# Kernel tuning notes

Hardware: AMD Instinct MI355X
Metric: run time of the kernel (lower is better)

## Reference

```python
import jax, jax.numpy as jnp
import numpy as np

B, HW, N, C, F, ITERS = 32, 4096, 16, 128, 512, 3
EPS_LN = 1e-5
EPS_ATTN = 1e-5


def _ln(x, g, b):
    m = x.mean(-1, keepdims=True)
    v = ((x - m) ** 2).mean(-1, keepdims=True)
    return (x - m) / jnp.sqrt(v + EPS_LN) * g + b


def _gru(x, h, wih, whh, bih, bhh):
    # torch.nn.GRUCell math
    gi = x @ wih.T + bih
    gh = h @ whh.T + bhh
    i_r, i_z, i_n = jnp.split(gi, 3, axis=-1)
    h_r, h_z, h_n = jnp.split(gh, 3, axis=-1)
    r = jax.nn.sigmoid(i_r + h_r)
    z = jax.nn.sigmoid(i_z + h_z)
    n = jnp.tanh(i_n + r * h_n)
    return (1.0 - z) * n + z * h


def setup_inputs() -> dict:
    key = jax.random.key(0)
    ks = jax.random.split(key, 16)
    s = 0.02
    d = {
        'inp': jax.random.normal(ks[0], (B, HW, C), jnp.float32),
        'query': jax.random.normal(ks[1], (B, N, C), jnp.float32),
        'ln_kv_g': jnp.ones((C,), jnp.float32),
        'ln_kv_b': jnp.zeros((C,), jnp.float32),
        'Wk': jax.random.normal(ks[2], (C, C), jnp.float32) * s,
        'Wv': jax.random.normal(ks[3], (C, C), jnp.float32) * s,
        'ln_q_g': jnp.ones((C,), jnp.float32),
        'ln_q_b': jnp.zeros((C,), jnp.float32),
        'Wq': jax.random.normal(ks[4], (C, C), jnp.float32) * s,
        'gru_wih': jax.random.normal(ks[5], (3 * C, C), jnp.float32) * s,
        'gru_whh': jax.random.normal(ks[6], (3 * C, C), jnp.float32) * s,
        'gru_bih': jnp.zeros((3 * C,), jnp.float32),
        'gru_bhh': jnp.zeros((3 * C,), jnp.float32),
        'ln2_g': jnp.ones((C,), jnp.float32),
        'ln2_b': jnp.zeros((C,), jnp.float32),
        'ffn_w1': jax.random.normal(ks[7], (F, C), jnp.float32) * s,
        'ffn_b1': jnp.zeros((F,), jnp.float32),
        'ffn_w2': jax.random.normal(ks[8], (C, F), jnp.float32) * s,
        'ffn_b2': jnp.zeros((C,), jnp.float32),
    }
    return d


def reference(inp, query, ln_kv_g, ln_kv_b, Wk, Wv, ln_q_g, ln_q_b, Wq,
              gru_wih, gru_whh, gru_bih, gru_bhh, ln2_g, ln2_b,
              ffn_w1, ffn_b1, ffn_w2, ffn_b2):
    b, n, c = query.shape
    kv = _ln(inp, ln_kv_g, ln_kv_b)
    k = kv @ Wk.T  # (b, hw, c)
    v = kv @ Wv.T  # (b, hw, c)
    scale = c ** -0.5
    q = query
    a0 = None
    for _ in range(ITERS):
        x = q
        qn = _ln(q, ln_q_g, ln_q_b) @ Wq.T
        logit = jnp.einsum('bqc,bkc->bqk', qn * scale, k)  # (b, n, hw)
        a0 = jax.nn.softmax(logit, axis=1)  # inverted: softmax over slots
        a = a0 / (a0.sum(2, keepdims=True) + EPS_ATTN)  # renorm over keys
        u = jnp.einsum('bqk,bkc->bqc', a, v)
        y = _gru(u.reshape(b * n, c), x.reshape(b * n, c),
                 gru_wih, gru_whh, gru_bih, gru_bhh).reshape(b, n, c)
        z = _ln(y, ln2_g, ln2_b)
        ffn = jax.nn.relu(z @ ffn_w1.T + ffn_b1) @ ffn_w2.T + ffn_b2
        q = y + ffn
    return (q, a0)
```

## Files before the change

kernel.cpp:

```cpp
#include <hip/hip_runtime.h>
#include <math.h>

#define B_ 32
#define HW_ 4096
#define N_ 16
#define C_ 128
#define F_ 512
#define ITERS_ 3
#define EPS_LN 1e-5f
#define EPS_ATTN 1e-5f

typedef __attribute__((ext_vector_type(8))) short short8;
typedef __attribute__((ext_vector_type(4))) float f32x4;

static __device__ __forceinline__ unsigned short f2b(float f) {
    union { float f; unsigned u; } v; v.f = f;
    unsigned r = v.u + 0x7fffu + ((v.u >> 16) & 1u);
    return (unsigned short)(r >> 16);
}
static __device__ __forceinline__ float blo(unsigned u) {
    union { unsigned u; float f; } v; v.u = u << 16; return v.f;
}
static __device__ __forceinline__ float bhi(unsigned u) {
    union { unsigned u; float f; } v; v.u = u & 0xffff0000u; return v.f;
}

__global__ __launch_bounds__(256) void k_wprep(
    const float* __restrict__ Wk, const float* __restrict__ Wv,
    const float* __restrict__ wih, const float* __restrict__ whh,
    const float* __restrict__ w1, const float* __restrict__ w2,
    unsigned short* __restrict__ Wk_bf, unsigned short* __restrict__ Wv_bf,
    unsigned short* __restrict__ wih_bf, unsigned short* __restrict__ whh_bf,
    unsigned short* __restrict__ w1_bf, unsigned short* __restrict__ w2_bf)
{
    int t = blockIdx.x * 256 + threadIdx.x;
    const float* src; unsigned short* dst; int off;
    if (t < 4096)       { src = Wk;  dst = Wk_bf;  off = t; }
    else if (t < 8192)  { src = Wv;  dst = Wv_bf;  off = t - 4096; }
    else if (t < 20480) { src = wih; dst = wih_bf; off = t - 8192; }
    else if (t < 32768) { src = whh; dst = whh_bf; off = t - 20480; }
    else if (t < 49152) { src = w1;  dst = w1_bf;  off = t - 32768; }
    else                { src = w2;  dst = w2_bf;  off = t - 49152; }
    float4 a = ((const float4*)src)[off];
    unsigned lo = (unsigned)f2b(a.x) | ((unsigned)f2b(a.y) << 16);
    unsigned hi = (unsigned)f2b(a.z) | ((unsigned)f2b(a.w) << 16);
    uint2 p; p.x = lo; p.y = hi;
    *(uint2*)(dst + off * 4) = p;
}

__global__ __launch_bounds__(256) void k_qprep0(
    const float* __restrict__ query, const float* __restrict__ lng,
    const float* __restrict__ lnb, const float* __restrict__ Wq,
    unsigned short* __restrict__ qn_g)
{
    __shared__ __align__(16) float xq[16 * 128];
    int b = blockIdx.x, tid = threadIdx.x;
    int n = tid >> 4, part = tid & 15;
    int row = b * 16 + n;
    const float4* x4 = (const float4*)(query + row * 128 + part * 8);
    float4 x0 = x4[0], x1 = x4[1];
    float s = x0.x + x0.y + x0.z + x0.w + x1.x + x1.y + x1.z + x1.w;
    float ss = x0.x * x0.x + x0.y * x0.y + x0.z * x0.z + x0.w * x0.w +
               x1.x * x1.x + x1.y * x1.y + x1.z * x1.z + x1.w * x1.w;
    s += __shfl_xor(s, 1); s += __shfl_xor(s, 2); s += __shfl_xor(s, 4); s += __shfl_xor(s, 8);
    ss += __shfl_xor(ss, 1); ss += __shfl_xor(ss, 2); ss += __shfl_xor(ss, 4); ss += __shfl_xor(ss, 8);
    float mean = s * (1.f / 128.f);
    float var = ss * (1.f / 128.f) - mean * mean;
    float rstd = rsqrtf(var + EPS_LN);
    const float4* g4 = (const float4*)(lng + part * 8);
    const float4* b4 = (const float4*)(lnb + part * 8);
    float4 g0 = g4[0], g1 = g4[1], bb0 = b4[0], bb1 = b4[1];
    float4 o0, o1;
    o0.x = (x0.x - mean) * rstd * g0.x + bb0.x;
    o0.y = (x0.y - mean) * rstd * g0.y + bb0.y;
    o0.z = (x0.z - mean) * rstd * g0.z + bb0.z;
    o0.w = (x0.w - mean) * rstd * g0.w + bb0.w;
    o1.x = (x1.x - mean) * rstd * g1.x + bb1.x;
    o1.y = (x1.y - mean) * rstd * g1.y + bb1.y;
    o1.z = (x1.z - mean) * rstd * g1.z + bb1.z;
    o1.w = (x1.w - mean) * rstd * g1.w + bb1.w;
    float4* xrow = (float4*)&xq[n * 128];
    xrow[part * 2] = o0;
    xrow[part * 2 + 1] = o1;
    __syncthreads();
    float o[8] = {0.f, 0.f, 0.f, 0.f, 0.f, 0.f, 0.f, 0.f};
    const float4* xv4 = (const float4*)&xq[n * 128];
#pragma unroll 4
    for (int j = 0; j < 32; j++) {
        float4 xv = xv4[j];
#pragma unroll
        for (int i = 0; i < 8; i++) {
            float4 w = ((const float4*)(Wq + (part * 8 + i) * 128))[j];
            o[i] += w.x * xv.x + w.y * xv.y + w.z * xv.z + w.w * xv.w;
        }
    }
    const float scale = 0.08838834764831845f;
#pragma unroll
    for (int i = 0; i < 8; i++)
        qn_g[row * 128 + part * 8 + i] = f2b(o[i] * scale);
}

__global__ __launch_bounds__(256) void k_kvproj(
    const float* __restrict__ inp, const float* __restrict__ lng,
    const float* __restrict__ lnb, const unsigned short* __restrict__ Wk_bf,
    const unsigned short* __restrict__ Wv_bf, unsigned short* __restrict__ Kbf,
    unsigned short* __restrict__ Vt)
{
    __shared__ __align__(16) unsigned short W_lds[128 * 128];
    __shared__ __align__(16) unsigned short T_lds[64 * 136];
    const int tid = threadIdx.x;
    const int wave = tid >> 6, lane = tid & 63;
    const int l15 = lane & 15, q4 = lane >> 4;
    const int kof = q4 * 8;
    const int tile0 = blockIdx.x * 64;
    const int b = tile0 >> 12;
    const int hwbase = tile0 & (HW_ - 1);

    const int srow = tid >> 1, shalf = tid & 1;
    const int sswz = srow & 7;

    float x[4][8];
    {
        const float* rowp = inp + (tile0 + (wave << 4) + l15) * C_;
        float s = 0.f, ss = 0.f;
#pragma unroll
        for (int ks = 0; ks < 4; ks++) {
#pragma unroll
            for (int h = 0; h < 2; h++) {
                float4 v = *(const float4*)(rowp + ks * 32 + kof + h * 4);
                x[ks][h * 4 + 0] = v.x; x[ks][h * 4 + 1] = v.y;
                x[ks][h * 4 + 2] = v.z; x[ks][h * 4 + 3] = v.w;
                s += v.x + v.y + v.z + v.w;
                ss += v.x * v.x + v.y * v.y + v.z * v.z + v.w * v.w;
            }
        }
        s += __shfl_xor(s, 16);  s += __shfl_xor(s, 32);
        ss += __shfl_xor(ss, 16); ss += __shfl_xor(ss, 32);
        float mean = s * (1.f / 128.f);
        float var = ss * (1.f / 128.f) - mean * mean;
        float rstd = rsqrtf(var + EPS_LN);
#pragma unroll
        for (int ks = 0; ks < 4; ks++) {
#pragma unroll
            for (int h = 0; h < 2; h++) {
                float4 g = *(const float4*)(lng + ks * 32 + kof + h * 4);
                float4 bb = *(const float4*)(lnb + ks * 32 + kof + h * 4);
                x[ks][h * 4 + 0] = (x[ks][h * 4 + 0] - mean) * rstd * g.x + bb.x;
                x[ks][h * 4 + 1] = (x[ks][h * 4 + 1] - mean) * rstd * g.y + bb.y;
                x[ks][h * 4 + 2] = (x[ks][h * 4 + 2] - mean) * rstd * g.z + bb.z;
                x[ks][h * 4 + 3] = (x[ks][h * 4 + 3] - mean) * rstd * g.w + bb.w;
            }
        }
    }
    short8 af[4];
#pragma unroll
    for (int ks = 0; ks < 4; ks++) {
        union { short8 s8; unsigned u[4]; } p;
#pragma unroll
        for (int j = 0; j < 4; j++)
            p.u[j] = (unsigned)f2b(x[ks][2 * j]) | ((unsigned)f2b(x[ks][2 * j + 1]) << 16);
        af[ks] = p.s8;
    }

    {
        const uint4* gW = (const uint4*)Wk_bf;
#pragma unroll
        for (int j = 0; j < 8; j++) {
            int c = shalf * 8 + j;
            uint4 w = gW[srow * 16 + c];
            *(uint4*)&W_lds[srow * 128 + (c ^ sswz) * 8] = w;
        }
    }
    __syncthreads();

    f32x4 acc[8];
#pragma unroll
    for (int nt = 0; nt < 8; nt++) {
        acc[nt] = (f32x4){0.f, 0.f, 0.f, 0.f};
#pragma unroll
        for (int ks = 0; ks < 4; ks++) {
            short8 bf = *(const short8*)&W_lds[(nt * 16 + l15) * 128 + ((ks * 4 + q4) ^ (l15 & 7)) * 8];
            acc[nt] = __builtin_amdgcn_mfma_f32_16x16x32_bf16(af[ks], bf, acc[nt], 0, 0, 0);
        }
    }
#pragma unroll
    for (int nt = 0; nt < 8; nt++) {
        int c = nt * 16 + l15;
#pragma unroll
        for (int i = 0; i < 4; i++)
            T_lds[((wave << 4) + (q4 << 2) + i) * 136 + c] = f2b(acc[nt][i]);
    }
    __syncthreads();
    {
        int row = tid >> 2, part = tid & 3;
        uint4 v0 = *(const uint4*)&T_lds[row * 136 + part * 32];
        uint4 v1 = *(const uint4*)&T_lds[row * 136 + part * 32 + 8];
        uint4* dst = (uint4*)&Kbf[(b * HW_ + hwbase + row) * C_ + part * 32];
        dst[0] = v0;
        dst[1] = v1;
    }
    {
        const uint4* gW = (const uint4*)Wv_bf;
#pragma unroll
        for (int j = 0; j < 8; j++) {
            int c = shalf * 8 + j;
            uint4 w = gW[srow * 16 + c];
            *(uint4*)&W_lds[srow * 128 + (c ^ sswz) * 8] = w;
        }
    }
    __syncthreads();
#pragma unroll
    for (int nt = 0; nt < 8; nt++) {
        acc[nt] = (f32x4){0.f, 0.f, 0.f, 0.f};
#pragma unroll
        for (int ks = 0; ks < 4; ks++) {
            short8 bf = *(const short8*)&W_lds[(nt * 16 + l15) * 128 + ((ks * 4 + q4) ^ (l15 & 7)) * 8];
            acc[nt] = __builtin_amdgcn_mfma_f32_16x16x32_bf16(af[ks], bf, acc[nt], 0, 0, 0);
        }
    }
#pragma unroll
    for (int nt = 0; nt < 8; nt++) {
        int c = nt * 16 + l15;
#pragma unroll
        for (int i = 0; i < 4; i++)
            T_lds[((wave << 4) + (q4 << 2) + i) * 136 + c] = f2b(acc[nt][i]);
    }
    __syncthreads();
    {
        int c = tid >> 1, half = tid & 1;
        unsigned short* vbase = Vt + (b * C_ + c) * HW_ + hwbase + half * 32;
#pragma unroll
        for (int g = 0; g < 4; g++) {
            union { uint4 u4; unsigned u[4]; } p;
#pragma unroll
            for (int d = 0; d < 4; d++) {
                int h = half * 32 + g * 8 + d * 2;
                unsigned lo = T_lds[h * 136 + c];
                unsigned hi = T_lds[(h + 1) * 136 + c];
                p.u[d] = lo | (hi << 16);
            }
            *(uint4*)(vbase + g * 8) = p.u4;
        }
    }
}

__global__ __launch_bounds__(256) void k_attn(
    const unsigned short* __restrict__ qn_g, const unsigned short* __restrict__ Kbf,
    const unsigned short* __restrict__ Vt, float* __restrict__ Upart,
    float* __restrict__ rspart, float* __restrict__ a0_out, int last)
{
    __shared__ __align__(16) float Ul[4][2048];
    __shared__ __align__(16) unsigned short Pb[4][16 * 40];
    __shared__ float rsw[4][16];
    const int b = blockIdx.y, chunk = blockIdx.x;
    const int tid = threadIdx.x;
    const int wave = tid >> 6, lane = tid & 63;
    const int l15 = lane & 15, q4 = lane >> 4;
    const int kof = q4 * 8;
    const int hwb = chunk * 128 + wave * 32;

    short8 aq[4];
#pragma unroll
    for (int ks = 0; ks < 4; ks++)
        aq[ks] = *(const short8*)&qn_g[(b * 16 + l15) * 128 + ks * 32 + kof];

    unsigned short* Pw = &Pb[wave][0];
    float rs[4] = {0.f, 0.f, 0.f, 0.f};
#pragma unroll
    for (int s = 0; s < 2; s++) {
        int hwt = hwb + s * 16;
        f32x4 sa = {0.f, 0.f, 0.f, 0.f};
#pragma unroll
        for (int ks = 0; ks < 4; ks++) {
            short8 bk = *(const short8*)&Kbf[(b * HW_ + hwt + l15) * C_ + ks * 32 + kof];
            sa = __builtin_amdgcn_mfma_f32_16x16x32_bf16(aq[ks], bk, sa, 0, 0, 0);
        }
        float mx = fmaxf(fmaxf(sa[0], sa[1]), fmaxf(sa[2], sa[3]));
        mx = fmaxf(mx, __shfl_xor(mx, 16));
        mx = fmaxf(mx, __shfl_xor(mx, 32));
        float e[4]; float ssum = 0.f;
#pragma unroll
        for (int i = 0; i < 4; i++) { e[i] = __expf(sa[i] - mx); ssum += e[i]; }
        ssum += __shfl_xor(ssum, 16);
        ssum += __shfl_xor(ssum, 32);
        float inv = 1.f / ssum;
#pragma unroll
        for (int i = 0; i < 4; i++) {
            float a0v = e[i] * inv;
            rs[i] += a0v;
            if (last) a0_out[(b * 16 + q4 * 4 + i) * HW_ + hwt + l15] = a0v;
            Pw[(q4 * 4 + i) * 40 + s * 16 + l15] = f2b(a0v);
        }
    }
#pragma unroll
    for (int i = 0; i < 4; i++) {
        rs[i] += __shfl_xor(rs[i], 1);
        rs[i] += __shfl_xor(rs[i], 2);
        rs[i] += __shfl_xor(rs[i], 4);
        rs[i] += __shfl_xor(rs[i], 8);
    }
    if (l15 == 0) {
#pragma unroll
        for (int i = 0; i < 4; i++) rsw[wave][q4 * 4 + i] = rs[i];
    }
    short8 bp = *(const short8*)&Pw[l15 * 40 + kof];
#pragma unroll
    for (int ct = 0; ct < 8; ct++) {
        short8 av = *(const short8*)&Vt[(b * C_ + ct * 16 + l15) * HW_ + hwb + kof];
        f32x4 ua = __builtin_amdgcn_mfma_f32_16x16x32_bf16(av, bp, (f32x4){0.f, 0.f, 0.f, 0.f}, 0, 0, 0);
        int c = ct * 16 + q4 * 4;
#pragma unroll
        for (int i = 0; i < 4; i++)
            Ul[wave][(c + i) * 16 + l15] = ua[i];
    }
    __syncthreads();
    {
        float* up = Upart + (b * 32 + chunk) * 2048;
#pragma unroll
        for (int k = 0; k < 8; k++) {
            int idx = tid + k * 256;
            up[idx] = Ul[0][idx] + Ul[1][idx] + Ul[2][idx] + Ul[3][idx];
        }
        if (tid < 16)
            rspart[(b * 32 + chunk) * 16 + tid] =
                rsw[0][tid] + rsw[1][tid] + rsw[2][tid] + rsw[3][tid];
    }
}

__global__ __launch_bounds__(256) void k_tail(
    const float* __restrict__ Upart, const float* __restrict__ rspart,
    const float* __restrict__ hsrc, float* __restrict__ q_buf,
    const unsigned short* __restrict__ wih_bf, const unsigned short* __restrict__ whh_bf,
    const float* __restrict__ bih, const float* __restrict__ bhh,
    const float* __restrict__ ln2g, const float* __restrict__ ln2b,
    const unsigned short* __restrict__ w1_bf, const float* __restrict__ b1,
    const unsigned short* __restrict__ w2_bf, const float* __restrict__ b2,
    const float* __restrict__ lnqg, const float* __restrict__ lnqb,
    const float* __restrict__ Wq, unsigned short* __restrict__ qn_g,
    float* __restrict__ out_q, int last)
{
    __shared__ __align__(16) float u_l[2][128];
    __shared__ __align__(16) float h_l[2][128];
    __shared__ __align__(16) float g_l[2][768];
    __shared__ __align__(16) float z_l[2][128];
    __shared__ __align__(16) float y_l[2][128];
    __shared__ __align__(16) float h1_l[2][512];
    __shared__ float stats[2][2];
    __shared__ float wpart[4][2];
    int tid = threadIdx.x;
    int row0 = blockIdx.x * 2;
    int r = tid >> 7, c = tid & 127;
    int row = row0 + r;
    {
        int bb = row >> 4, q = row & 15;
        float rsv = 0.f, uraw = 0.f;
#pragma unroll
        for (int ch = 0; ch < 32; ch++) {
            rsv  += rspart[(bb * 32 + ch) * 16 + q];
            uraw += Upart[(bb * 32 + ch) * 2048 + c * 16 + q];
        }
        u_l[r][c] = uraw / (rsv + EPS_ATTN);
        h_l[r][c] = hsrc[row * 128 + c];
    }
    __syncthreads();
#pragma unroll
    for (int o3 = 0; o3 < 3; o3++) {
        int o = tid + o3 * 256;
        const unsigned short* wrow;
        const float* srcbase;
        float bias;
        if (o < 384) { wrow = wih_bf + o * 128; srcbase = &u_l[0][0]; bias = bih[o]; }
        else         { wrow = whh_bf + (o - 384) * 128; srcbase = &h_l[0][0]; bias = bhh[o - 384]; }
        const uint4* w4 = (const uint4*)wrow;
        const float4* s0 = (const float4*)srcbase;
        const float4* s1 = (const float4*)(srcbase + 128);
        float a0acc = 0.f, a1acc = 0.f;
#pragma unroll 8
        for (int j = 0; j < 16; j++) {
            uint4 w = w4[j];
            float w0 = blo(w.x), w1v = bhi(w.x), w2v = blo(w.y), w3 = bhi(w.y);
            float w4v = blo(w.z), w5 = bhi(w.z), w6 = blo(w.w), w7 = bhi(w.w);
            float4 aA = s0[2 * j], aB = s0[2 * j + 1];
            float4 bA = s1[2 * j], bB = s1[2 * j + 1];
            a0acc += w0 * aA.x + w1v * aA.y + w2v * aA.z + w3 * aA.w
                   + w4v * aB.x + w5 * aB.y + w6 * aB.z + w7 * aB.w;
            a1acc += w0 * bA.x + w1v * bA.y + w2v * bA.z + w3 * bA.w
                   + w4v * bB.x + w5 * bB.y + w6 * bB.z + w7 * bB.w;
        }
        g_l[0][o] = a0acc + bias;
        g_l[1][o] = a1acc + bias;
    }
    __syncthreads();
    {
        float ir = g_l[r][c], iz = g_l[r][128 + c], in_ = g_l[r][256 + c];
        float hr = g_l[r][384 + c], hz = g_l[r][512 + c], hn = g_l[r][640 + c];
        float rr = 1.f / (1.f + expf(-(ir + hr)));
        float zz = 1.f / (1.f + expf(-(iz + hz)));
        float nn = tanhf(in_ + rr * hn);
        y_l[r][c] = (1.f - zz) * nn + zz * h_l[r][c];
    }
    __syncthreads();
    if (tid < 128) {
        int w = tid >> 6, ln = tid & 63;
        float v0 = y_l[w][ln], v1 = y_l[w][ln + 64];
        float s = v0 + v1, ss = v0 * v0 + v1 * v1;
#pragma unroll
        for (int off = 1; off < 64; off <<= 1) {
            s += __shfl_xor(s, off);
            ss += __shfl_xor(ss, off);
        }
        if (ln == 0) {
            float mean = s * (1.f / 128.f);
            float var = ss * (1.f / 128.f) - mean * mean;
            stats[w][0] = mean;
            stats[w][1] = rsqrtf(var + EPS_LN);
        }
    }
    __syncthreads();
    z_l[r][c] = (y_l[r][c] - stats[r][0]) * stats[r][1] * ln2g[c] + ln2b[c];
    __syncthreads();
#pragma unroll
    for (int f2i = 0; f2i < 2; f2i++) {
        int f = tid + f2i * 256;
        const uint4* w4 = (const uint4*)(w1_bf + f * 128);
        const float4* s0 = (const float4*)&z_l[0][0];
        const float4* s1 = (const float4*)&z_l[1][0];
        float a0acc = 0.f, a1acc = 0.f;
#pragma unroll 8
        for (int j = 0; j < 16; j++) {
            uint4 w = w4[j];
            float w0 = blo(w.x), w1v = bhi(w.x), w2v = blo(w.y), w3 = bhi(w.y);
            float w4v = blo(w.z), w5 = bhi(w.z), w6 = blo(w.w), w7 = bhi(w.w);
            float4 aA = s0[2 * j], aB = s0[2 * j + 1];
            float4 bA = s1[2 * j], bB = s1[2 * j + 1];
            a0acc += w0 * aA.x + w1v * aA.y + w2v * aA.z + w3 * aA.w
                   + w4v * aB.x + w5 * aB.y + w6 * aB.z + w7 * aB.w;
            a1acc += w0 * bA.x + w1v * bA.y + w2v * bA.z + w3 * bA.w
                   + w4v * bB.x + w5 * bB.y + w6 * bB.z + w7 * bB.w;
        }
        float bv = b1[f];
        h1_l[0][f] = fmaxf(a0acc + bv, 0.f);
        h1_l[1][f] = fmaxf(a1acc + bv, 0.f);
    }
    __syncthreads();
    float q_new;
    {
        const uint4* w4 = (const uint4*)(w2_bf + c * 512);
        const float4* hh = (const float4*)&h1_l[r][0];
        float acc = 0.f;
#pragma unroll 8
        for (int j = 0; j < 64; j++) {
            uint4 w = w4[j];
            float4 hA = hh[2 * j], hB = hh[2 * j + 1];
            acc += blo(w.x) * hA.x + bhi(w.x) * hA.y + blo(w.y) * hA.z + bhi(w.y) * hA.w
                 + blo(w.z) * hB.x + bhi(w.z) * hB.y + blo(w.w) * hB.z + bhi(w.w) * hB.w;
        }
        q_new = y_l[r][c] + acc + b2[c];
        q_buf[row * 128 + c] = q_new;
        if (last) out_q[row * 128 + c] = q_new;
    }
    if (!last) {
        __syncthreads();
        y_l[r][c] = q_new;
        __syncthreads();
        {
            int w = tid >> 6, ln = tid & 63;
            float v = y_l[w >> 1][(w & 1) * 64 + ln];
            float s = v, ss = v * v;
#pragma unroll
            for (int off = 1; off < 64; off <<= 1) {
                s += __shfl_xor(s, off);
                ss += __shfl_xor(ss, off);
            }
            if (ln == 0) { wpart[w][0] = s; wpart[w][1] = ss; }
        }
        __syncthreads();
        {
            float s = wpart[2 * r][0] + wpart[2 * r + 1][0];
            float ss = wpart[2 * r][1] + wpart[2 * r + 1][1];
            float mean = s * (1.f / 128.f);
            float var = ss * (1.f / 128.f) - mean * mean;
            float rstd = rsqrtf(var + EPS_LN);
            z_l[r][c] = (q_new - mean) * rstd * lnqg[c] + lnqb[c];
        }
        __syncthreads();
        {
            const float4* w4 = (const float4*)(Wq + c * 128);
            const float4* zz = (const float4*)&z_l[r][0];
            float acc = 0.f;
#pragma unroll 8
            for (int j = 0; j < 32; j++) {
                float4 w = w4[j], v = zz[j];
                acc += w.x * v.x + w.y * v.y + w.z * v.z + w.w * v.w;
            }
            qn_g[row * 128 + c] = f2b(acc * 0.08838834764831845f);
        }
    }
}

extern "C" void kernel_launch(void* const* d_in, const int* in_sizes, int n_in,
                              void* d_out, int out_size, void* d_ws, size_t ws_size,
                              hipStream_t stream) {
    const float* inp     = (const float*)d_in[0];
    const float* query   = (const float*)d_in[1];
    const float* ln_kv_g = (const float*)d_in[2];
    const float* ln_kv_b = (const float*)d_in[3];
    const float* Wk      = (const float*)d_in[4];
    const float* Wv      = (const float*)d_in[5];
    const float* ln_q_g  = (const float*)d_in[6];
    const float* ln_q_b  = (const float*)d_in[7];
    const float* Wq      = (const float*)d_in[8];
    const float* gru_wih = (const float*)d_in[9];
    const float* gru_whh = (const float*)d_in[10];
    const float* gru_bih = (const float*)d_in[11];
    const float* gru_bhh = (const float*)d_in[12];
    const float* ln2_g   = (const float*)d_in[13];
    const float* ln2_b   = (const float*)d_in[14];
    const float* ffn_w1  = (const float*)d_in[15];
    const float* ffn_b1  = (const float*)d_in[16];
    const float* ffn_w2  = (const float*)d_in[17];
    const float* ffn_b2  = (const float*)d_in[18];

    char* ws = (char*)d_ws;
    unsigned short* Kbf    = (unsigned short*)ws;
    unsigned short* Vt     = (unsigned short*)(ws + 33554432);
    float* q_buf           = (float*)(ws + 67108864);
    float* Upart           = (float*)(ws + 67371008);
    float* rspart          = (float*)(ws + 75759616);
    unsigned short* qn_g   = (unsigned short*)(ws + 75825152);
    unsigned short* Wk_bf  = (unsigned short*)(ws + 75956224);
    unsigned short* Wv_bf  = (unsigned short*)(ws + 75988992);
    unsigned short* wih_bf = (unsigned short*)(ws + 76021760);
    unsigned short* whh_bf = (unsigned short*)(ws + 76120064);
    unsigned short* w1_bf  = (unsigned short*)(ws + 76218368);
    unsigned short* w2_bf  = (unsigned short*)(ws + 76349440);

    float* out_q  = (float*)d_out;
    float* out_a0 = out_q + B_ * N_ * C_;

    k_wprep<<<dim3(256), dim3(256), 0, stream>>>(
        Wk, Wv, gru_wih, gru_whh, ffn_w1, ffn_w2,
        Wk_bf, Wv_bf, wih_bf, whh_bf, w1_bf, w2_bf);
    k_qprep0<<<dim3(B_), dim3(256), 0, stream>>>(query, ln_q_g, ln_q_b, Wq, qn_g);
    k_kvproj<<<dim3((B_ * HW_) / 64), dim3(256), 0, stream>>>(
        inp, ln_kv_g, ln_kv_b, Wk_bf, Wv_bf, Kbf, Vt);

    for (int it = 0; it < ITERS_; it++) {
        int last = (it == ITERS_ - 1) ? 1 : 0;
        const float* hsrc = (it == 0) ? query : q_buf;
        k_attn<<<dim3(32, B_), dim3(256), 0, stream>>>(
            qn_g, Kbf, Vt, Upart, rspart, out_a0, last);
        k_tail<<<dim3((B_ * N_) / 2), dim3(256), 0, stream>>>(
            Upart, rspart, hsrc, q_buf, wih_bf, whh_bf, gru_bih, gru_bhh,
            ln2_g, ln2_b, w1_bf, ffn_b1, w2_bf, ffn_b2,
            ln_q_g, ln_q_b, Wq, qn_g, out_q, last);
    }
}
```

Before: 342.3 us.

## Merge prep kernels, transpose V via LDS, prefetch V in attention, one row per tail block

Fuses the weight-conversion and initial query-projection kernels into one launch. In the KV projection, V is now staged in LDS already transposed, so the Vt store uses vector copies instead of gathering scalar 16-bit values. The K staging uses a different row pitch. The attention kernel loads its V fragments before the score computation and reuses the U buffer for P, which drops an LDS array. The tail kernel now gives each block a single row, doubling the grid, and splits reductions across both halves of the block. This adds parallelism but also adds extra barriers and reads each weight matrix twice as often.

```diff
diff --git a/kernel.cpp b/kernel.cpp
--- a/kernel.cpp
+++ b/kernel.cpp
@@ -25,36 +25,36 @@
     union { unsigned u; float f; } v; v.u = u & 0xffff0000u; return v.f;
 }
 
-__global__ __launch_bounds__(256) void k_wprep(
+__global__ __launch_bounds__(256) void k_prep(
     const float* __restrict__ Wk, const float* __restrict__ Wv,
     const float* __restrict__ wih, const float* __restrict__ whh,
     const float* __restrict__ w1, const float* __restrict__ w2,
     unsigned short* __restrict__ Wk_bf, unsigned short* __restrict__ Wv_bf,
     unsigned short* __restrict__ wih_bf, unsigned short* __restrict__ whh_bf,
-    unsigned short* __restrict__ w1_bf, unsigned short* __restrict__ w2_bf)
-{
-    int t = blockIdx.x * 256 + threadIdx.x;
-    const float* src; unsigned short* dst; int off;
-    if (t < 4096)       { src = Wk;  dst = Wk_bf;  off = t; }
-    else if (t < 8192)  { src = Wv;  dst = Wv_bf;  off = t - 4096; }
-    else if (t < 20480) { src = wih; dst = wih_bf; off = t - 8192; }
-    else if (t < 32768) { src = whh; dst = whh_bf; off = t - 20480; }
-    else if (t < 49152) { src = w1;  dst = w1_bf;  off = t - 32768; }
-    else                { src = w2;  dst = w2_bf;  off = t - 49152; }
-    float4 a = ((const float4*)src)[off];
-    unsigned lo = (unsigned)f2b(a.x) | ((unsigned)f2b(a.y) << 16);
-    unsigned hi = (unsigned)f2b(a.z) | ((unsigned)f2b(a.w) << 16);
-    uint2 p; p.x = lo; p.y = hi;
-    *(uint2*)(dst + off * 4) = p;
-}
-
-__global__ __launch_bounds__(256) void k_qprep0(
-    const float* __restrict__ query, const float* __restrict__ lng,
-    const float* __restrict__ lnb, const float* __restrict__ Wq,
+    unsigned short* __restrict__ w1_bf, unsigned short* __restrict__ w2_bf,
+    const float* __restrict__ query, const float* __restrict__ lnqg,
+    const float* __restrict__ lnqb, const float* __restrict__ Wq,
     unsigned short* __restrict__ qn_g)
 {
     __shared__ __align__(16) float xq[16 * 128];
-    int b = blockIdx.x, tid = threadIdx.x;
+    int tid = threadIdx.x;
+    if (blockIdx.x < 256) {
+        int t = blockIdx.x * 256 + tid;
+        const float* src; unsigned short* dst; int off;
+        if (t < 4096)       { src = Wk;  dst = Wk_bf;  off = t; }
+        else if (t < 8192)  { src = Wv;  dst = Wv_bf;  off = t - 4096; }
+        else if (t < 20480) { src = wih; dst = wih_bf; off = t - 8192; }
+        else if (t < 32768) { src = whh; dst = whh_bf; off = t - 20480; }
+        else if (t < 49152) { src = w1;  dst = w1_bf;  off = t - 32768; }
+        else                { src = w2;  dst = w2_bf;  off = t - 49152; }
+        float4 a = ((const float4*)src)[off];
+        uint2 p;
+        p.x = (unsigned)f2b(a.x) | ((unsigned)f2b(a.y) << 16);
+        p.y = (unsigned)f2b(a.z) | ((unsigned)f2b(a.w) << 16);
+        *(uint2*)(dst + off * 4) = p;
+        return;
+    }
+    int b = blockIdx.x - 256;
     int n = tid >> 4, part = tid & 15;
     int row = b * 16 + n;
     const float4* x4 = (const float4*)(query + row * 128 + part * 8);
@@ -67,8 +67,8 @@
     float mean = s * (1.f / 128.f);
     float var = ss * (1.f / 128.f) - mean * mean;
     float rstd = rsqrtf(var + EPS_LN);
-    const float4* g4 = (const float4*)(lng + part * 8);
-    const float4* b4 = (const float4*)(lnb + part * 8);
+    const float4* g4 = (const float4*)(lnqg + part * 8);
+    const float4* b4 = (const float4*)(lnqb + part * 8);
     float4 g0 = g4[0], g1 = g4[1], bb0 = b4[0], bb1 = b4[1];
     float4 o0, o1;
     o0.x = (x0.x - mean) * rstd * g0.x + bb0.x;
@@ -107,7 +107,7 @@
     unsigned short* __restrict__ Vt)
 {
     __shared__ __align__(16) unsigned short W_lds[128 * 128];
-    __shared__ __align__(16) unsigned short T_lds[64 * 136];
+    __shared__ __align__(16) unsigned short T_lds[8960];
     const int tid = threadIdx.x;
     const int wave = tid >> 6, lane = tid & 63;
     const int l15 = lane & 15, q4 = lane >> 4;
@@ -188,16 +188,15 @@
         int c = nt * 16 + l15;
 #pragma unroll
         for (int i = 0; i < 4; i++)
-            T_lds[((wave << 4) + (q4 << 2) + i) * 136 + c] = f2b(acc[nt][i]);
+            T_lds[((wave << 4) + (q4 << 2) + i) * 132 + c] = f2b(acc[nt][i]);
     }
     __syncthreads();
     {
         int row = tid >> 2, part = tid & 3;
-        uint4 v0 = *(const uint4*)&T_lds[row * 136 + part * 32];
-        uint4 v1 = *(const uint4*)&T_lds[row * 136 + part * 32 + 8];
         uint4* dst = (uint4*)&Kbf[(b * HW_ + hwbase + row) * C_ + part * 32];
-        dst[0] = v0;
-        dst[1] = v1;
+#pragma unroll
+        for (int j = 0; j < 4; j++)
+            dst[j] = *(const uint4*)&T_lds[row * 132 + part * 32 + j * 8];
     }
     {
         const uint4* gW = (const uint4*)Wv_bf;
@@ -218,29 +217,21 @@
             acc[nt] = __builtin_amdgcn_mfma_f32_16x16x32_bf16(af[ks], bf, acc[nt], 0, 0, 0);
         }
     }
+    __syncthreads();
 #pragma unroll
     for (int nt = 0; nt < 8; nt++) {
         int c = nt * 16 + l15;
 #pragma unroll
         for (int i = 0; i < 4; i++)
-            T_lds[((wave << 4) + (q4 << 2) + i) * 136 + c] = f2b(acc[nt][i]);
+            T_lds[c * 70 + (wave << 4) + (q4 << 2) + i] = f2b(acc[nt][i]);
     }
     __syncthreads();
     {
         int c = tid >> 1, half = tid & 1;
-        unsigned short* vbase = Vt + (b * C_ + c) * HW_ + hwbase + half * 32;
-#pragma unroll
-        for (int g = 0; g < 4; g++) {
-            union { uint4 u4; unsigned u[4]; } p;
-#pragma unroll
-            for (int d = 0; d < 4; d++) {
-                int h = half * 32 + g * 8 + d * 2;
-                unsigned lo = T_lds[h * 136 + c];
-                unsigned hi = T_lds[(h + 1) * 136 + c];
-                p.u[d] = lo | (hi << 16);
-            }
-            *(uint4*)(vbase + g * 8) = p.u4;
-        }
+        uint4* dst = (uint4*)&Vt[(b * C_ + c) * HW_ + hwbase + half * 32];
+#pragma unroll
+        for (int j = 0; j < 4; j++)
+            dst[j] = *(const uint4*)&T_lds[c * 70 + half * 32 + j * 8];
     }
 }
 
@@ -250,7 +241,6 @@
     float* __restrict__ rspart, float* __restrict__ a0_out, int last)
 {
     __shared__ __align__(16) float Ul[4][2048];
-    __shared__ __align__(16) unsigned short Pb[4][16 * 40];
     __shared__ float rsw[4][16];
     const int b = blockIdx.y, chunk = blockIdx.x;
     const int tid = threadIdx.x;
@@ -259,12 +249,17 @@
     const int kof = q4 * 8;
     const int hwb = chunk * 128 + wave * 32;
 
+    unsigned short* Pw = (unsigned short*)&Ul[wave][0];
+
     short8 aq[4];
 #pragma unroll
     for (int ks = 0; ks < 4; ks++)
         aq[ks] = *(const short8*)&qn_g[(b * 16 + l15) * 128 + ks * 32 + kof];
-
-    unsigned short* Pw = &Pb[wave][0];
+    short8 av[8];
+#pragma unroll
+    for (int ct = 0; ct < 8; ct++)
+        av[ct] = *(const short8*)&Vt[(b * C_ + ct * 16 + l15) * HW_ + hwb + kof];
+
     float rs[4] = {0.f, 0.f, 0.f, 0.f};
 #pragma unroll
     for (int s = 0; s < 2; s++) {
@@ -306,8 +301,7 @@
     short8 bp = *(const short8*)&Pw[l15 * 40 + kof];
 #pragma unroll
     for (int ct = 0; ct < 8; ct++) {
-        short8 av = *(const short8*)&Vt[(b * C_ + ct * 16 + l15) * HW_ + hwb + kof];
-        f32x4 ua = __builtin_amdgcn_mfma_f32_16x16x32_bf16(av, bp, (f32x4){0.f, 0.f, 0.f, 0.f}, 0, 0, 0);
+        f32x4 ua = __builtin_amdgcn_mfma_f32_16x16x32_bf16(av[ct], bp, (f32x4){0.f, 0.f, 0.f, 0.f}, 0, 0, 0);
         int c = ct * 16 + q4 * 4;
 #pragma unroll
         for (int i = 0; i < 4; i++)
@@ -339,162 +333,164 @@
     const float* __restrict__ Wq, unsigned short* __restrict__ qn_g,
     float* __restrict__ out_q, int last)
 {
-    __shared__ __align__(16) float u_l[2][128];
-    __shared__ __align__(16) float h_l[2][128];
-    __shared__ __align__(16) float g_l[2][768];
-    __shared__ __align__(16) float z_l[2][128];
-    __shared__ __align__(16) float y_l[2][128];
-    __shared__ __align__(16) float h1_l[2][512];
-    __shared__ float stats[2][2];
-    __shared__ float wpart[4][2];
-    int tid = threadIdx.x;
-    int row0 = blockIdx.x * 2;
-    int r = tid >> 7, c = tid & 127;
-    int row = row0 + r;
-    {
-        int bb = row >> 4, q = row & 15;
-        float rsv = 0.f, uraw = 0.f;
-#pragma unroll
-        for (int ch = 0; ch < 32; ch++) {
-            rsv  += rspart[(bb * 32 + ch) * 16 + q];
-            uraw += Upart[(bb * 32 + ch) * 2048 + c * 16 + q];
-        }
-        u_l[r][c] = uraw / (rsv + EPS_ATTN);
-        h_l[r][c] = hsrc[row * 128 + c];
-    }
+    __shared__ __align__(16) float u_l[128];
+    __shared__ __align__(16) float h_l[128];
+    __shared__ __align__(16) float g_l[768];
+    __shared__ __align__(16) float z_l[128];
+    __shared__ __align__(16) float y_l[128];
+    __shared__ __align__(16) float h1_l[512];
+    __shared__ __align__(16) float red[256];
+    __shared__ float stats[2];
+    __shared__ float srs;
+    const int tid = threadIdx.x;
+    const int row = blockIdx.x;
+    const int b = row >> 4, q = row & 15;
+    const int lane = tid & 63;
+
+    {
+        int c = tid & 127, h = tid >> 7;
+        float part = 0.f;
+#pragma unroll
+        for (int ch = 0; ch < 16; ch++)
+            part += Upart[(b * 32 + h * 16 + ch) * 2048 + c * 16 + q];
+        red[tid] = part;
+        if (tid < 128) h_l[tid] = hsrc[row * 128 + tid];
+        if (tid < 64) {
+            float v = (lane < 32) ? rspart[(b * 32 + lane) * 16 + q] : 0.f;
+#pragma unroll
+            for (int off = 1; off < 64; off <<= 1) v += __shfl_xor(v, off);
+            if (tid == 0) srs = v;
+        }
+    }
+    __syncthreads();
+    if (tid < 128)
+        u_l[tid] = (red[tid] + red[tid + 128]) / (srs + EPS_ATTN);
     __syncthreads();
 #pragma unroll
     for (int o3 = 0; o3 < 3; o3++) {
         int o = tid + o3 * 256;
         const unsigned short* wrow;
-        const float* srcbase;
+        const float* src;
         float bias;
-        if (o < 384) { wrow = wih_bf + o * 128; srcbase = &u_l[0][0]; bias = bih[o]; }
-        else         { wrow = whh_bf + (o - 384) * 128; srcbase = &h_l[0][0]; bias = bhh[o - 384]; }
+        if (o < 384) { wrow = wih_bf + o * 128; src = u_l; bias = bih[o]; }
+        else         { wrow = whh_bf + (o - 384) * 128; src = h_l; bias = bhh[o - 384]; }
         const uint4* w4 = (const uint4*)wrow;
-        const float4* s0 = (const float4*)srcbase;
-        const float4* s1 = (const float4*)(srcbase + 128);
-        float a0acc = 0.f, a1acc = 0.f;
+        const float4* s4 = (const float4*)src;
+        float acc = 0.f;
 #pragma unroll 8
         for (int j = 0; j < 16; j++) {
             uint4 w = w4[j];
-            float w0 = blo(w.x), w1v = bhi(w.x), w2v = blo(w.y), w3 = bhi(w.y);
-            float w4v = blo(w.z), w5 = bhi(w.z), w6 = blo(w.w), w7 = bhi(w.w);
-            float4 aA = s0[2 * j], aB = s0[2 * j + 1];
-            float4 bA = s1[2 * j], bB = s1[2 * j + 1];
-            a0acc += w0 * aA.x + w1v * aA.y + w2v * aA.z + w3 * aA.w
-                   + w4v * aB.x + w5 * aB.y + w6 * aB.z + w7 * aB.w;
-            a1acc += w0 * bA.x + w1v * bA.y + w2v * bA.z + w3 * bA.w
-                   + w4v * bB.x + w5 * bB.y + w6 * bB.z + w7 * bB.w;
-        }
-        g_l[0][o] = a0acc + bias;
-        g_l[1][o] = a1acc + bias;
-    }
-    __syncthreads();
-    {
-        float ir = g_l[r][c], iz = g_l[r][128 + c], in_ = g_l[r][256 + c];
-        float hr = g_l[r][384 + c], hz = g_l[r][512 + c], hn = g_l[r][640 + c];
+            float4 aA = s4[2 * j], aB = s4[2 * j + 1];
+            acc += blo(w.x) * aA.x + bhi(w.x) * aA.y + blo(w.y) * aA.z + bhi(w.y) * aA.w
+                 + blo(w.z) * aB.x + bhi(w.z) * aB.y + blo(w.w) * aB.z + bhi(w.w) * aB.w;
+        }
+        g_l[o] = acc + bias;
+    }
+    __syncthreads();
+    if (tid < 128) {
+        int c = tid;
+        float ir = g_l[c], iz = g_l[128 + c], in_ = g_l[256 + c];
+        float hr = g_l[384 + c], hz = g_l[512 + c], hn = g_l[640 + c];
         float rr = 1.f / (1.f + expf(-(ir + hr)));
         float zz = 1.f / (1.f + expf(-(iz + hz)));
         float nn = tanhf(in_ + rr * hn);
-        y_l[r][c] = (1.f - zz) * nn + zz * h_l[r][c];
-    }
-    __syncthreads();
-    if (tid < 128) {
-        int w = tid >> 6, ln = tid & 63;
-        float v0 = y_l[w][ln], v1 = y_l[w][ln + 64];
+        y_l[c] = (1.f - zz) * nn + zz * h_l[c];
+    }
+    __syncthreads();
+    if (tid < 64) {
+        float v0 = y_l[lane], v1 = y_l[lane + 64];
         float s = v0 + v1, ss = v0 * v0 + v1 * v1;
 #pragma unroll
         for (int off = 1; off < 64; off <<= 1) {
             s += __shfl_xor(s, off);
             ss += __shfl_xor(ss, off);
         }
-        if (ln == 0) {
+        if (tid == 0) {
             float mean = s * (1.f / 128.f);
             float var = ss * (1.f / 128.f) - mean * mean;
-            stats[w][0] = mean;
-            stats[w][1] = rsqrtf(var + EPS_LN);
-        }
-    }
-    __syncthreads();
-    z_l[r][c] = (y_l[r][c] - stats[r][0]) * stats[r][1] * ln2g[c] + ln2b[c];
+            stats[0] = mean;
+            stats[1] = rsqrtf(var + EPS_LN);
+        }
+    }
+    __syncthreads();
+    if (tid < 128)
+        z_l[tid] = (y_l[tid] - stats[0]) * stats[1] * ln2g[tid] + ln2b[tid];
     __syncthreads();
 #pragma unroll
     for (int f2i = 0; f2i < 2; f2i++) {
         int f = tid + f2i * 256;
         const uint4* w4 = (const uint4*)(w1_bf + f * 128);
-        const float4* s0 = (const float4*)&z_l[0][0];
-        const float4* s1 = (const float4*)&z_l[1][0];
-        float a0acc = 0.f, a1acc = 0.f;
+        const float4* s4 = (const float4*)z_l;
+        float acc = 0.f;
 #pragma unroll 8
         for (int j = 0; j < 16; j++) {
             uint4 w = w4[j];
-            float w0 = blo(w.x), w1v = bhi(w.x), w2v = blo(w.y), w3 = bhi(w.y);
-            float w4v = blo(w.z), w5 = bhi(w.z), w6 = blo(w.w), w7 = bhi(w.w);
-            float4 aA = s0[2 * j], aB = s0[2 * j + 1];
-            float4 bA = s1[2 * j], bB = s1[2 * j + 1];
-            a0acc += w0 * aA.x + w1v * aA.y + w2v * aA.z + w3 * aA.w
-                   + w4v * aB.x + w5 * aB.y + w6 * aB.z + w7 * aB.w;
-            a1acc += w0 * bA.x + w1v * bA.y + w2v * bA.z + w3 * bA.w
-                   + w4v * bB.x + w5 * bB.y + w6 * bB.z + w7 * bB.w;
-        }
-        float bv = b1[f];
-        h1_l[0][f] = fmaxf(a0acc + bv, 0.f);
-        h1_l[1][f] = fmaxf(a1acc + bv, 0.f);
-    }
-    __syncthreads();
-    float q_new;
-    {
-        const uint4* w4 = (const uint4*)(w2_bf + c * 512);
-        const float4* hh = (const float4*)&h1_l[r][0];
+            float4 aA = s4[2 * j], aB = s4[2 * j + 1];
+            acc += blo(w.x) * aA.x + bhi(w.x) * aA.y + blo(w.y) * aA.z + bhi(w.y) * aA.w
+                 + blo(w.z) * aB.x + bhi(w.z) * aB.y + blo(w.w) * aB.z + bhi(w.w) * aB.w;
+        }
+        h1_l[f] = fmaxf(acc + b1[f], 0.f);
+    }
+    __syncthreads();
+    {
+        int c = tid & 127, h = tid >> 7;
+        const uint4* w4 = (const uint4*)(w2_bf + c * 512 + h * 256);
+        const float4* hh = (const float4*)&h1_l[h * 256];
         float acc = 0.f;
 #pragma unroll 8
-        for (int j = 0; j < 64; j++) {
+        for (int j = 0; j < 32; j++) {
             uint4 w = w4[j];
             float4 hA = hh[2 * j], hB = hh[2 * j + 1];
             acc += blo(w.x) * hA.x + bhi(w.x) * hA.y + blo(w.y) * hA.z + bhi(w.y) * hA.w
                  + blo(w.z) * hB.x + bhi(w.z) * hB.y + blo(w.w) * hB.z + bhi(w.w) * hB.w;
         }
-        q_new = y_l[r][c] + acc + b2[c];
-        q_buf[row * 128 + c] = q_new;
-        if (last) out_q[row * 128 + c] = q_new;
+        red[tid] = acc;
+    }
+    __syncthreads();
+    float q_new = 0.f;
+    if (tid < 128) {
+        q_new = y_l[tid] + red[tid] + red[tid + 128] + b2[tid];
+        q_buf[row * 128 + tid] = q_new;
+        if (last) out_q[row * 128 + tid] = q_new;
     }
     if (!last) {
         __syncthreads();
-        y_l[r][c] = q_new;
+        if (tid < 128) y_l[tid] = q_new;
         __syncthreads();
-        {
-            int w = tid >> 6, ln = tid & 63;
-            float v = y_l[w >> 1][(w & 1) * 64 + ln];
-            float s = v, ss = v * v;
+        if (tid < 64) {
+            float v0 = y_l[lane], v1 = y_l[lane + 64];
+            float s = v0 + v1, ss = v0 * v0 + v1 * v1;
 #pragma unroll
             for (int off = 1; off < 64; off <<= 1) {
                 s += __shfl_xor(s, off);
                 ss += __shfl_xor(ss, off);
             }
-            if (ln == 0) { wpart[w][0] = s; wpart[w][1] = ss; }
-        }
+            if (tid == 0) {
+                float mean = s * (1.f / 128.f);
+                float var = ss * (1.f / 128.f) - mean * mean;
+                stats[0] = mean;
+                stats[1] = rsqrtf(var + EPS_LN);
+            }
+        }
+        __syncthreads();
+        if (tid < 128)
+            z_l[tid] = (y_l[tid] - stats[0]) * stats[1] * lnqg[tid] + lnqb[tid];
         __syncthreads();
         {
-            float s = wpart[2 * r][0] + wpart[2 * r + 1][0];
-            float ss = wpart[2 * r][1] + wpart[2 * r + 1][1];
-            float mean = s * (1.f / 128.f);
-            float var = ss * (1.f / 128.f) - mean * mean;
-            float rstd = rsqrtf(var + EPS_LN);
-            z_l[r][c] = (q_new - mean) * rstd * lnqg[c] + lnqb[c];
-        }
-        __syncthreads();
-        {
-            const float4* w4 = (const float4*)(Wq + c * 128);
-            const float4* zz = (const float4*)&z_l[r][0];
+            int c = tid & 127, h = tid >> 7;
+            const float4* w4 = (const float4*)(Wq + c * 128 + h * 64);
+            const float4* zz = (const float4*)&z_l[h * 64];
             float acc = 0.f;
 #pragma unroll 8
-            for (int j = 0; j < 32; j++) {
+            for (int j = 0; j < 16; j++) {
                 float4 w = w4[j], v = zz[j];
                 acc += w.x * v.x + w.y * v.y + w.z * v.z + w.w * v.w;
             }
-            qn_g[row * 128 + c] = f2b(acc * 0.08838834764831845f);
-        }
+            red[tid] = acc;
+        }
+        __syncthreads();
+        if (tid < 128)
+            qn_g[row * 128 + tid] = f2b((red[tid] + red[tid + 128]) * 0.08838834764831845f);
     }
 }
 
@@ -538,10 +534,10 @@
     float* out_q  = (float*)d_out;
     float* out_a0 = out_q + B_ * N_ * C_;
 
-    k_wprep<<<dim3(256), dim3(256), 0, stream>>>(
+    k_prep<<<dim3(288), dim3(256), 0, stream>>>(
         Wk, Wv, gru_wih, gru_whh, ffn_w1, ffn_w2,
-        Wk_bf, Wv_bf, wih_bf, whh_bf, w1_bf, w2_bf);
-    k_qprep0<<<dim3(B_), dim3(256), 0, stream>>>(query, ln_q_g, ln_q_b, Wq, qn_g);
+        Wk_bf, Wv_bf, wih_bf, whh_bf, w1_bf, w2_bf,
+        query, ln_q_g, ln_q_b, Wq, qn_g);
     k_kvproj<<<dim3((B_ * HW_) / 64), dim3(256), 0, stream>>>(
         inp, ln_kv_g, ln_kv_b, Wk_bf, Wv_bf, Kbf, Vt);
 
@@ -550,7 +546,7 @@
         const float* hsrc = (it == 0) ? query : q_buf;
         k_attn<<<dim3(32, B_), dim3(256), 0, stream>>>(
             qn_g, Kbf, Vt, Upart, rspart, out_a0, last);
-        k_tail<<<dim3((B_ * N_) / 2), dim3(256), 0, stream>>>(
+        k_tail<<<dim3(B_ * N_), dim3(256), 0, stream>>>(
             Upart, rspart, hsrc, q_buf, wih_bf, whh_bf, gru_bih, gru_bhh,
             ln2_g, ln2_b, w1_bf, ffn_b1, w2_bf, ffn_b2,
             ln_q_g, ln_q_b, Wq, qn_g, out_q, last);
```

New measurement: 350.4 us. 1.02x slower.
